# Optimization experiments

Hardware: AMD Instinct MI355X
Metric: run time of the kernel (lower is better)

The kernel has to match this reference:

```python
import jax, jax.numpy as jnp
import numpy as np
import math

D_MODEL = 1024
N_HEADS = 16
HEAD_DIM = D_MODEL // N_HEADS
FEAT = 16
WINDOW = 64
EPS_NORM = 1e-6
EPS_LIN = 1e-6
CHUNK = 128


def setup_inputs() -> dict:
    key = jax.random.key(0)
    ks = jax.random.split(key, 7)
    B, T = 2, 2048
    s = 0.02
    return {
        'x': jax.random.normal(ks[0], (B, T, D_MODEL), jnp.float32),
        'norm_w': jnp.ones((D_MODEL,), jnp.float32),
        'Wq': jax.random.normal(ks[1], (D_MODEL, D_MODEL), jnp.float32) * s,
        'Wk': jax.random.normal(ks[2], (D_MODEL, D_MODEL), jnp.float32) * s,
        'Wv': jax.random.normal(ks[3], (D_MODEL, D_MODEL), jnp.float32) * s,
        'Wqf': jax.random.normal(ks[4], (HEAD_DIM, FEAT), jnp.float32) * s,
        'Wkf': jax.random.normal(ks[5], (HEAD_DIM, FEAT), jnp.float32) * s,
        'Wout': jax.random.normal(ks[6], (2 * D_MODEL, D_MODEL), jnp.float32) * s,
    }


def rmsnorm(x, w):
    return x * jax.lax.rsqrt(jnp.mean(x * x, axis=-1, keepdims=True) + EPS_NORM) * w


def taylor_feature_map(x):
    # phi(x) = [1, x, x_i*x_j * (0.5 if i==j else 1/sqrt(2)) for i<=j]
    d = x.shape[-1]
    iu, ju = jnp.triu_indices(d)  # row-major (i, j>=i) matches torch loop order
    scale = jnp.where(iu == ju, 0.5, 1.0 / math.sqrt(2.0)).astype(x.dtype)
    quad = x[..., iu] * x[..., ju] * scale
    ones = jnp.ones(x.shape[:-1] + (1,), dtype=x.dtype)
    return jnp.concatenate([ones, x, quad], axis=-1)  # (..., 1+d+d(d+1)/2)


def linear_attention_causal(q_phi, k_phi, v):
    # Chunked-parallel causal linear attention: y_t = q_t @ KV_t / (q_t @ Ksum_t + eps)
    B, T, H, F = q_phi.shape
    D = v.shape[-1]
    Nc = T // CHUNK
    qc = q_phi.reshape(B, Nc, CHUNK, H, F).transpose(1, 0, 2, 3, 4)  # (Nc,B,C,H,F)
    kc = k_phi.reshape(B, Nc, CHUNK, H, F).transpose(1, 0, 2, 3, 4)
    vc = v.reshape(B, Nc, CHUNK, H, D).transpose(1, 0, 2, 3, 4)      # (Nc,B,C,H,D)
    causal = jnp.tril(jnp.ones((CHUNK, CHUNK), dtype=q_phi.dtype))   # include diagonal

    def step(carry, inp):
        kv, ksum = carry                      # (B,H,F,D), (B,H,F)
        qb, kb, vb = inp
        A = jnp.einsum('bchf,bshf->bhcs', qb, kb) * causal  # intra-chunk quadratic scores
        y = jnp.einsum('bhcs,bshd->bchd', A, vb) + jnp.einsum('bchf,bhfd->bchd', qb, kv)
        z = jnp.einsum('bhcs->bch', A) + jnp.einsum('bchf,bhf->bch', qb, ksum)
        kv = kv + jnp.einsum('bshf,bshd->bhfd', kb, vb)
        ksum = ksum + kb.sum(axis=1)
        return (kv, ksum), y / (z[..., None] + EPS_LIN)

    kv0 = jnp.zeros((B, H, F, D), dtype=q_phi.dtype)
    ks0 = jnp.zeros((B, H, F), dtype=q_phi.dtype)
    _, ys = jax.lax.scan(step, (kv0, ks0), (qc, kc, vc))
    return ys.transpose(1, 0, 2, 3, 4).reshape(B, T, H, D)


def sliding_window_attention(q, k, v):
    B, T, H, D = q.shape
    scale = 1.0 / math.sqrt(D)
    t = jnp.arange(T)
    allowed = (t[None, :] <= t[:, None]) & (t[None, :] >= t[:, None] - WINDOW)  # (T,T)
    scores = jnp.einsum('bqhd,bkhd->bhqk', q, k) * scale
    scores = jnp.where(allowed[None, None], scores, -jnp.inf)
    attn = jax.nn.softmax(scores, axis=-1)
    out = jnp.einsum('bhqk,bkhd->bqhd', attn, v)
    return out.reshape(B, T, H * D)


def reference(x, norm_w, Wq, Wk, Wv, Wqf, Wkf, Wout):
    B, T, _ = x.shape
    h = rmsnorm(x, norm_w)
    q = (h @ Wq).reshape(B, T, N_HEADS, HEAD_DIM)
    k = (h @ Wk).reshape(B, T, N_HEADS, HEAD_DIM)
    v = (h @ Wv).reshape(B, T, N_HEADS, HEAD_DIM)
    q_phi = taylor_feature_map(q @ Wqf)
    k_phi = taylor_feature_map(k @ Wkf)
    lin = linear_attention_causal(q_phi, k_phi, v).reshape(B, T, D_MODEL)
    win = sliding_window_attention(q, k, v)
    out = jnp.concatenate([lin, win], axis=-1) @ Wout
    return x + out
```

## Files before the change

kernel.cpp:

```cpp
#include <hip/hip_runtime.h>
#include <math.h>

#define BB 2
#define TT 2048
#define DM 1024
#define NH 16
#define HD 64
#define FEAT 16
#define WIN 64
#define RTOT (BB*TT)

typedef __bf16 bf16x8 __attribute__((ext_vector_type(8)));
typedef float  f32x4  __attribute__((ext_vector_type(4)));

__device__ __forceinline__ unsigned short f2bf(float f) {
    union { float f; unsigned u; } v; v.f = f;
    unsigned r = v.u + 0x7FFFu + ((v.u >> 16) & 1u);
    return (unsigned short)(r >> 16);
}
__device__ __forceinline__ float bf2f(unsigned short u) {
    union { unsigned u; float f; } v; v.u = ((unsigned)u) << 16; return v.f;
}

__device__ __forceinline__ void gl2lds16(const void* g, void* l) {
    __builtin_amdgcn_global_load_lds(
        (const __attribute__((address_space(1))) void*)g,
        (__attribute__((address_space(3))) void*)l, 16, 0, 0);
}

__global__ __launch_bounds__(256) void rmsnorm_kernel(const float* __restrict__ x,
                                                      const float* __restrict__ w,
                                                      unsigned short* __restrict__ h_bf) {
    int row = blockIdx.x;
    int tid = threadIdx.x;
    const float4* xr = (const float4*)(x + (size_t)row * DM);
    float4 xv = xr[tid];
    float ss = xv.x*xv.x + xv.y*xv.y + xv.z*xv.z + xv.w*xv.w;
    #pragma unroll
    for (int off = 32; off > 0; off >>= 1) ss += __shfl_down(ss, off, 64);
    __shared__ float red[4];
    if ((tid & 63) == 0) red[tid >> 6] = ss;
    __syncthreads();
    float tot = red[0] + red[1] + red[2] + red[3];
    float scale = rsqrtf(tot * (1.0f / DM) + 1e-6f);
    float4 wv = ((const float4*)w)[tid];
    ushort4 o;
    o.x = f2bf(xv.x * scale * wv.x);
    o.y = f2bf(xv.y * scale * wv.y);
    o.z = f2bf(xv.z * scale * wv.z);
    o.w = f2bf(xv.w * scale * wv.w);
    *(ushort4*)&h_bf[(size_t)row * DM + tid * 4] = o;
}

__global__ __launch_bounds__(256) void transpose_bf16_kernel(const float* __restrict__ W0,
                                                             const float* __restrict__ W1,
                                                             const float* __restrict__ W2,
                                                             const float* __restrict__ W3,
                                                             unsigned short* __restrict__ T0,
                                                             unsigned short* __restrict__ T1,
                                                             unsigned short* __restrict__ T2,
                                                             unsigned short* __restrict__ T3) {
    int z = blockIdx.z;
    int K = (z == 3) ? 2048 : 1024;
    const int N = 1024;
    if (blockIdx.y * 64 >= K) return;
    const float* W = (z == 0) ? W0 : (z == 1) ? W1 : (z == 2) ? W2 : W3;
    unsigned short* WT = (z == 0) ? T0 : (z == 1) ? T1 : (z == 2) ? T2 : T3;
    __shared__ float tile[64][65];
    int k0 = blockIdx.y * 64, n0 = blockIdx.x * 64;
    int t = threadIdx.x;
    int r = t >> 4, c4 = (t & 15) * 4;
    #pragma unroll
    for (int i = 0; i < 4; i++) {
        float4 vv = *(const float4*)&W[(size_t)(k0 + r + i*16) * N + n0 + c4];
        tile[r + i*16][c4 + 0] = vv.x;
        tile[r + i*16][c4 + 1] = vv.y;
        tile[r + i*16][c4 + 2] = vv.z;
        tile[r + i*16][c4 + 3] = vv.w;
    }
    __syncthreads();
    int rn = t >> 2, kq = (t & 3) * 16;
    unsigned short u[16];
    #pragma unroll
    for (int i = 0; i < 16; i++) u[i] = f2bf(tile[kq + i][rn]);
    size_t base = (size_t)(n0 + rn) * K + k0 + kq;
    *(uint4*)&WT[base]     = *(uint4*)&u[0];
    *(uint4*)&WT[base + 8] = *(uint4*)&u[8];
}

template<int LD, int NT>
__device__ __forceinline__ void gemm2h_core(const unsigned short* __restrict__ A,
                                            const unsigned short* __restrict__ BT,
                                            unsigned short* __restrict__ Cb,
                                            int k0g) {
    const int N = 1024;
    __shared__ __align__(16) unsigned short L[2][4][256 * 32];
    int tid = threadIdx.x;
    int lane = tid & 63;
    int w = tid >> 6;
    int wm = (w >> 2) * 128, wn = (w & 3) * 64;
    int m0 = blockIdx.y * 256, n0 = blockIdx.x * 256;
    int hi = lane >> 4;
    int l15 = lane & 15;

    int c0 = tid, c1 = tid + 512;
    int r0 = c0 >> 2, kh0 = ((c0 & 3) - (r0 >> 1)) & 3;
    int r1 = c1 >> 2, kh1 = ((c1 & 3) - (r1 >> 1)) & 3;
    const unsigned short* aS0 = A  + (size_t)(m0 + r0) * LD + k0g + kh0 * 8;
    const unsigned short* aS1 = A  + (size_t)(m0 + r1) * LD + k0g + kh1 * 8;
    const unsigned short* bS0 = BT + (size_t)(n0 + r0) * LD + k0g + kh0 * 8;
    const unsigned short* bS1 = BT + (size_t)(n0 + r1) * LD + k0g + kh1 * 8;

    int aoff[8], boff[4];
    #pragma unroll
    for (int i = 0; i < 8; i++) {
        int m = wm + i * 16 + l15;
        aoff[i] = m * 32 + (((hi + (m >> 1)) & 3) * 8);
    }
    #pragma unroll
    for (int j = 0; j < 4; j++) {
        int n = wn + j * 16 + l15;
        boff[j] = n * 32 + (((hi + (n >> 1)) & 3) * 8);
    }

    f32x4 acc[8][4];
    #pragma unroll
    for (int i = 0; i < 8; i++)
        #pragma unroll
        for (int j = 0; j < 4; j++)
            acc[i][j] = (f32x4){0.f, 0.f, 0.f, 0.f};

#define STG8(kt, bf, rg) do {                                         \
        int _go = (kt) * 64 + ((rg) >> 1) * 32;                       \
        unsigned short* _d = &L[bf][rg][0];                           \
        if ((rg) & 1) { gl2lds16(bS0 + _go, _d + c0 * 8);             \
                        gl2lds16(bS1 + _go, _d + c1 * 8); }           \
        else          { gl2lds16(aS0 + _go, _d + c0 * 8);             \
                        gl2lds16(aS1 + _go, _d + c1 * 8); }           \
    } while (0)

    STG8(0, 0, 0); STG8(0, 0, 1); STG8(0, 0, 2); STG8(0, 0, 3);
    asm volatile("s_waitcnt vmcnt(4)" ::: "memory");
    __builtin_amdgcn_s_barrier();

    for (int t = 0; t < NT; t++) {
        int rd = t & 1, st = rd ^ 1;
        bool stg = (t + 1 < NT);
        const unsigned short* A0 = &L[rd][0][0];
        const unsigned short* B0 = &L[rd][1][0];
        const unsigned short* A1 = &L[rd][2][0];
        const unsigned short* B1 = &L[rd][3][0];
        bf16x8 af[8], bfr[4];

        asm volatile("" ::: "memory");
        #pragma unroll
        for (int i = 0; i < 8; i++) af[i] = *(const bf16x8*)&A0[aoff[i]];
        #pragma unroll
        for (int j = 0; j < 4; j++) bfr[j] = *(const bf16x8*)&B0[boff[j]];
        if (stg) { STG8(t + 1, st, 0); STG8(t + 1, st, 1); }
        __builtin_amdgcn_s_setprio(1);
        #pragma unroll
        for (int i = 0; i < 8; i++)
            #pragma unroll
            for (int j = 0; j < 4; j++)
                acc[i][j] = __builtin_amdgcn_mfma_f32_16x16x32_bf16(af[i], bfr[j], acc[i][j], 0, 0, 0);
        __builtin_amdgcn_s_setprio(0);
        if (stg) {
            asm volatile("s_waitcnt vmcnt(4)" ::: "memory");
        } else {
            asm volatile("s_waitcnt vmcnt(0)" ::: "memory");
        }
        __builtin_amdgcn_s_barrier();

        asm volatile("" ::: "memory");
        #pragma unroll
        for (int i = 0; i < 8; i++) af[i] = *(const bf16x8*)&A1[aoff[i]];
        #pragma unroll
        for (int j = 0; j < 4; j++) bfr[j] = *(const bf16x8*)&B1[boff[j]];
        if (stg) { STG8(t + 1, st, 2); STG8(t + 1, st, 3); }
        __builtin_amdgcn_s_setprio(1);
        #pragma unroll
        for (int i = 0; i < 8; i++)
            #pragma unroll
            for (int j = 0; j < 4; j++)
                acc[i][j] = __builtin_amdgcn_mfma_f32_16x16x32_bf16(af[i], bfr[j], acc[i][j], 0, 0, 0);
        __builtin_amdgcn_s_setprio(0);
        if (stg) {
            asm volatile("s_waitcnt vmcnt(4)" ::: "memory");
            __builtin_amdgcn_s_barrier();
        }
    }
#undef STG8

    #pragma unroll
    for (int i = 0; i < 8; i++) {
        #pragma unroll
        for (int j = 0; j < 4; j++) {
            int col = n0 + wn + j * 16 + l15;
            #pragma unroll
            for (int r = 0; r < 4; r++) {
                int row = m0 + wm + i * 16 + hi * 4 + r;
                Cb[(size_t)row * N + col] = f2bf(acc[i][j][r]);
            }
        }
    }
}

__global__ __launch_bounds__(512, 2) void gemm_qkv_mfma(const unsigned short* __restrict__ A,
                                                        const unsigned short* __restrict__ BT0,
                                                        const unsigned short* __restrict__ BT1,
                                                        const unsigned short* __restrict__ BT2,
                                                        unsigned short* __restrict__ C0,
                                                        unsigned short* __restrict__ C1,
                                                        unsigned short* __restrict__ C2) {
    const unsigned short* BT = (blockIdx.z == 0) ? BT0 : (blockIdx.z == 1) ? BT1 : BT2;
    unsigned short* C = (blockIdx.z == 0) ? C0 : (blockIdx.z == 1) ? C1 : C2;
    gemm2h_core<1024, 16>(A, BT, C, 0);
}

__global__ __launch_bounds__(512, 2) void gemm_out_mfma(const unsigned short* __restrict__ A,
                                                        const unsigned short* __restrict__ BT,
                                                        unsigned short* __restrict__ P0,
                                                        unsigned short* __restrict__ P1,
                                                        unsigned short* __restrict__ P2,
                                                        unsigned short* __restrict__ P3) {
    unsigned short* P = (blockIdx.z == 0) ? P0 : (blockIdx.z == 1) ? P1
                      : (blockIdx.z == 2) ? P2 : P3;
    gemm2h_core<2048, 8>(A, BT, P, blockIdx.z * 512);
}

__global__ __launch_bounds__(256) void out_reduce_kernel(const float* __restrict__ x,
                                                         const unsigned short* __restrict__ P0,
                                                         const unsigned short* __restrict__ P1,
                                                         const unsigned short* __restrict__ P2,
                                                         const unsigned short* __restrict__ P3,
                                                         float* __restrict__ out) {
    int g = blockIdx.x * 256 + threadIdx.x;
    size_t e = (size_t)g * 4;
    float4 xv = *(const float4*)&x[e];
    ushort4 a = *(const ushort4*)&P0[e];
    ushort4 b = *(const ushort4*)&P1[e];
    ushort4 c = *(const ushort4*)&P2[e];
    ushort4 d = *(const ushort4*)&P3[e];
    float4 o;
    o.x = xv.x + bf2f(a.x) + bf2f(b.x) + bf2f(c.x) + bf2f(d.x);
    o.y = xv.y + bf2f(a.y) + bf2f(b.y) + bf2f(c.y) + bf2f(d.y);
    o.z = xv.z + bf2f(a.z) + bf2f(b.z) + bf2f(c.z) + bf2f(d.z);
    o.w = xv.w + bf2f(a.w) + bf2f(b.w) + bf2f(c.w) + bf2f(d.w);
    *(float4*)&out[e] = o;
}

__global__ __launch_bounds__(256) void feat_kernel(const unsigned short* __restrict__ qb,
                                                   const unsigned short* __restrict__ kb,
                                                   const float* __restrict__ Wqf,
                                                   const float* __restrict__ Wkf,
                                                   unsigned short* __restrict__ qf,
                                                   unsigned short* __restrict__ kf) {
    __shared__ float Wl[HD * FEAT];
    const unsigned short* src = blockIdx.z ? kb : qb;
    const float* Wm = blockIdx.z ? Wkf : Wqf;
    unsigned short* dst = blockIdx.z ? kf : qf;
    int tid = threadIdx.x;
    ((float4*)Wl)[tid] = ((const float4*)Wm)[tid];
    __syncthreads();
    int gid = blockIdx.x * 256 + tid;
    int f = gid & 15;
    int rowh = gid >> 4;
    const unsigned short* s = src + (size_t)rowh * HD;
    float acc = 0.f;
    #pragma unroll
    for (int d = 0; d < HD; d++) acc += bf2f(s[d]) * Wl[d * FEAT + f];
    dst[gid] = f2bf(acc);
}

__global__ __launch_bounds__(256) void win_mfma_kernel(const unsigned short* __restrict__ q_bf,
                                                       const unsigned short* __restrict__ k_bf,
                                                       const unsigned short* __restrict__ v_bf,
                                                       unsigned short* __restrict__ cat_bf) {
    int qtile = blockIdx.x;
    int bh = blockIdx.y;
    int h = bh & 15;
    int b = bh >> 4;
    int tid = threadIdx.x;
    int lane = tid & 63;
    int wv = tid >> 6;
    int qr0 = wv * 16;
    int t0 = qtile * 64;
    int k0 = t0 - 64;

    __shared__ __align__(16) unsigned short Qs[64 * 64];
    __shared__ __align__(16) unsigned short Ks[128 * 64];
    __shared__ __align__(16) unsigned short Vt[64 * 128];
    __shared__ __align__(16) unsigned short Pl[64 * 128];

    #pragma unroll
    for (int half = 0; half < 2; half++) {
        int slot = tid + half * 256;
        int row = slot >> 3, pos = slot & 7;
        int o = (pos - row) & 7;
        gl2lds16(q_bf + (size_t)(b * TT + t0 + row) * (NH * HD) + h * HD + o * 8,
                 &Qs[slot * 8]);
    }
    #pragma unroll
    for (int qd = 0; qd < 4; qd++) {
        int slot = tid + qd * 256;
        int row = slot >> 3, pos = slot & 7;
        int o = (pos - row) & 7;
        int kg = k0 + row;
        if (kg >= 0) {
            gl2lds16(k_bf + (size_t)(b * TT + kg) * (NH * HD) + h * HD + o * 8,
                     &Ks[slot * 8]);
        } else {
            uint4 z = {0, 0, 0, 0};
            *(uint4*)&Ks[slot * 8] = z;
        }
    }
    {
        int kk = tid & 127;
        int dh = tid >> 7;
        int kg = k0 + kk;
        unsigned short tmp[32];
        if (kg >= 0) {
            size_t base = (size_t)(b * TT + kg) * (NH * HD) + h * HD + dh * 32;
            *(uint4*)&tmp[0]  = *(const uint4*)&v_bf[base];
            *(uint4*)&tmp[8]  = *(const uint4*)&v_bf[base + 8];
            *(uint4*)&tmp[16] = *(const uint4*)&v_bf[base + 16];
            *(uint4*)&tmp[24] = *(const uint4*)&v_bf[base + 24];
        } else {
            #pragma unroll
            for (int d = 0; d < 32; d++) tmp[d] = 0;
        }
        int o = kk >> 3, klow = kk & 7;
        #pragma unroll
        for (int d = 0; d < 32; d++) {
            int dim = dh * 32 + d;
            Vt[dim * 128 + ((o + dim) & 15) * 8 + klow] = tmp[d];
        }
    }
    __syncthreads();

    int hi = lane >> 4;
    int lan15 = lane & 15;
    f32x4 sc[8];
    #pragma unroll
    for (int nt = 0; nt < 8; nt++) sc[nt] = (f32x4){0.f, 0.f, 0.f, 0.f};
    #pragma unroll
    for (int ks = 0; ks < 2; ks++) {
        int m = qr0 + lan15;
        int oA = ks * 4 + hi;
        bf16x8 a = *(const bf16x8*)&Qs[m * 64 + ((oA + m) & 7) * 8];
        #pragma unroll
        for (int nt = 0; nt < 8; nt++) {
            int n = nt * 16 + lan15;
            bf16x8 bb = *(const bf16x8*)&Ks[n * 64 + ((oA + n) & 7) * 8];
            sc[nt] = __builtin_amdgcn_mfma_f32_16x16x32_bf16(a, bb, sc[nt], 0, 0, 0);
        }
    }

    float lrow[4];
    #pragma unroll
    for (int r = 0; r < 4; r++) {
        int tq = t0 + qr0 + hi * 4 + r;
        float mx = -1e30f;
        #pragma unroll
        for (int nt = 0; nt < 8; nt++) {
            int s = k0 + nt * 16 + lan15;
            bool ok = (s >= 0) && (s <= tq) && (s >= tq - WIN);
            float vv = ok ? sc[nt][r] * 0.125f : -1e30f;
            sc[nt][r] = vv;
            mx = fmaxf(mx, vv);
        }
        #pragma unroll
        for (int off = 1; off < 16; off <<= 1) mx = fmaxf(mx, __shfl_xor(mx, off, 64));
        float ls = 0.f;
        #pragma unroll
        for (int nt = 0; nt < 8; nt++) {
            float e = __expf(sc[nt][r] - mx);
            sc[nt][r] = e;
            ls += e;
        }
        #pragma unroll
        for (int off = 1; off < 16; off <<= 1) ls += __shfl_xor(ls, off, 64);
        lrow[r] = ls;
    }

    #pragma unroll
    for (int nt = 0; nt < 8; nt++) {
        #pragma unroll
        for (int r = 0; r < 4; r++) {
            int row = qr0 + hi * 4 + r;
            int col = nt * 16 + lan15;
            Pl[row * 128 + (((col >> 3) + row) & 15) * 8 + (col & 7)] = f2bf(sc[nt][r]);
        }
    }
    __syncthreads();

    f32x4 y[4];
    #pragma unroll
    for (int nt = 0; nt < 4; nt++) y[nt] = (f32x4){0.f, 0.f, 0.f, 0.f};
    #pragma unroll
    for (int ks = 0; ks < 4; ks++) {
        int m = qr0 + lan15;
        int oA = ks * 4 + hi;
        bf16x8 a = *(const bf16x8*)&Pl[m * 128 + ((oA + m) & 15) * 8];
        #pragma unroll
        for (int nt = 0; nt < 4; nt++) {
            int n = nt * 16 + lan15;
            bf16x8 bb = *(const bf16x8*)&Vt[n * 128 + ((oA + n) & 15) * 8];
            y[nt] = __builtin_amdgcn_mfma_f32_16x16x32_bf16(a, bb, y[nt], 0, 0, 0);
        }
    }

    #pragma unroll
    for (int nt = 0; nt < 4; nt++) {
        #pragma unroll
        for (int r = 0; r < 4; r++) {
            int row = qr0 + hi * 4 + r;
            int dim = nt * 16 + lan15;
            cat_bf[(size_t)(b * TT + t0 + row) * (2 * DM) + DM + h * HD + dim] =
                f2bf(y[nt][r] / lrow[r]);
        }
    }
}

#define PHI 160
#define NCH 32
#define KVROWS 65
#define CH_STRIDE ((size_t)32 * KVROWS * PHI)

__global__ __launch_bounds__(256) void lin_kv_kernel(const unsigned short* __restrict__ kf,
                                                     const unsigned short* __restrict__ v_bf,
                                                     unsigned short* __restrict__ kvbuf) {
    int c = blockIdx.x, bh = blockIdx.y;
    int h = bh & 15, b = bh >> 4;
    int tid = threadIdx.x, lane = tid & 63, w = tid >> 6;
    int hi = lane >> 4, l15 = lane & 15;

    __shared__ unsigned short kf_l[64 * 16];
    __shared__ __align__(16) unsigned short PhiT[192 * 76];
    __shared__ __align__(16) unsigned short Vt[80 * 64];
    __shared__ unsigned short iu[136], ju[136];
    __shared__ float sclut[136];

    if (tid < 136) {
        int qq = tid, i = 0;
        while (qq >= 16 - i) { qq -= 16 - i; i++; }
        iu[tid] = (unsigned short)i; ju[tid] = (unsigned short)(i + qq);
        sclut[tid] = (qq == 0) ? 0.5f : 0.70710678118654752f;
    }
    {
        int r = tid >> 2, f4 = (tid & 3) * 4;
        *(ushort4*)&kf_l[r * 16 + f4] =
            *(const ushort4*)&kf[((size_t)((b * TT + c * 64 + r) * NH + h)) * FEAT + f4];
    }
    {
        int p = tid & 31, dq = (tid >> 5) * 8;
        size_t base0 = ((size_t)(b * TT + c * 64 + 2 * p)) * DM + h * HD + dq;
        unsigned short a[8], bq[8];
        *(uint4*)a  = *(const uint4*)&v_bf[base0];
        *(uint4*)bq = *(const uint4*)&v_bf[base0 + DM];
        int colo = p >> 2, coll = (2 * p) & 7;
        #pragma unroll
        for (int d = 0; d < 8; d++) {
            int row = dq + d;
            ushort2 u; u.x = a[d]; u.y = bq[d];
            *(ushort2*)&Vt[row * 64 + ((colo + row) & 7) * 8 + coll] = u;
        }
        #pragma unroll
        for (int i = 0; i < 4; i++) {
            int e = tid + i * 256;
            Vt[(64 + (e >> 6)) * 64 + (e & 63)] = 0x3F80;
        }
    }
    __syncthreads();
    {
        int s = tid & 63, fb = tid >> 6;
        const unsigned short* krow = &kf_l[s * 16];
        for (int it = 0; it < 40; it++) {
            int f = fb * 40 + it;
            float val;
            if (f == 0) val = 1.f;
            else if (f < 17) val = bf2f(krow[f - 1]);
            else if (f < 153) { int qq = f - 17; val = bf2f(krow[iu[qq]]) * bf2f(krow[ju[qq]]) * sclut[qq]; }
            else val = 0.f;
            PhiT[f * 76 + s] = f2bf(val);
        }
    }
    __syncthreads();
    f32x4 acc[5][3];
    #pragma unroll
    for (int m = 0; m < 5; m++)
        #pragma unroll
        for (int j = 0; j < 3; j++) acc[m][j] = (f32x4){0.f, 0.f, 0.f, 0.f};
    #pragma unroll
    for (int ks = 0; ks < 2; ks++) {
        bf16x8 bfrag[3];
        #pragma unroll
        for (int j = 0; j < 3; j++)
            bfrag[j] = *(const bf16x8*)&PhiT[((3 * w + j) * 16 + l15) * 76 + ks * 32 + hi * 8];
        #pragma unroll
        for (int m = 0; m < 5; m++) {
            int mrow = m * 16 + l15;
            bf16x8 afrag = *(const bf16x8*)&Vt[mrow * 64 + (((ks * 4 + hi) + mrow) & 7) * 8];
            #pragma unroll
            for (int j = 0; j < 3; j++)
                acc[m][j] = __builtin_amdgcn_mfma_f32_16x16x32_bf16(afrag, bfrag[j], acc[m][j], 0, 0, 0);
        }
    }
    size_t obase = ((size_t)c * 32 + bh) * (KVROWS * PHI);
    #pragma unroll
    for (int m = 0; m < 5; m++) {
        #pragma unroll
        for (int j = 0; j < 3; j++) {
            int f = (3 * w + j) * 16 + l15;
            if (f >= PHI) continue;
            #pragma unroll
            for (int r = 0; r < 4; r++) {
                int row = m * 16 + hi * 4 + r;
                if (row >= KVROWS) continue;
                kvbuf[obase + row * PHI + f] = f2bf(acc[m][j][r]);
            }
        }
    }
}

__global__ __launch_bounds__(256) void lin_scan_kernel(unsigned short* __restrict__ kvbuf) {
    int e = blockIdx.x * 256 + threadIdx.x;
    int bh = blockIdx.y;
    if (e >= KVROWS * PHI) return;
    float acc = 0.f;
    size_t off = (size_t)bh * (KVROWS * PHI) + e;
    for (int c = 0; c < NCH; c++) {
        float vv = bf2f(kvbuf[off]);
        kvbuf[off] = f2bf(acc);
        acc += vv;
        off += CH_STRIDE;
    }
}

__global__ __launch_bounds__(256) void lin_out_kernel(const unsigned short* __restrict__ qf,
                                                      const unsigned short* __restrict__ kf,
                                                      const unsigned short* __restrict__ v_bf,
                                                      const unsigned short* __restrict__ kvbuf,
                                                      unsigned short* __restrict__ cat_bf) {
    int c = blockIdx.x, bh = blockIdx.y;
    int h = bh & 15, b = bh >> 4;
    int tid = threadIdx.x, lane = tid & 63, w = tid >> 6;
    int hi = lane >> 4, l15 = lane & 15;

    __shared__ unsigned short qf_l[64 * 16];
    __shared__ __align__(16) unsigned short kf_lb[64 * 34];
    __shared__ __align__(16) unsigned short KVS_l[80 * 164];
    __shared__ __align__(16) unsigned short Vt[80 * 64];
    __shared__ __align__(16) unsigned short Phi_l[64 * 164];
    __shared__ __align__(16) unsigned short P_l[64 * 64];
    __shared__ unsigned short iu[136], ju[136];
    __shared__ float sclut[136];

    if (tid < 136) {
        int qq = tid, i = 0;
        while (qq >= 16 - i) { qq -= 16 - i; i++; }
        iu[tid] = (unsigned short)i; ju[tid] = (unsigned short)(i + qq);
        sclut[tid] = (qq == 0) ? 0.5f : 0.70710678118654752f;
    }
    {
        int r = tid >> 2, f4 = (tid & 3) * 4;
        *(ushort4*)&qf_l[r * 16 + f4] =
            *(const ushort4*)&qf[((size_t)((b * TT + c * 64 + r) * NH + h)) * FEAT + f4];
    }
    {
        int r = tid >> 2, f4 = (tid & 3) * 4;
        *(ushort4*)&kf_lb[r * 34 + f4] =
            *(const ushort4*)&kf[((size_t)((b * TT + c * 64 + r) * NH + h)) * FEAT + f4];
        ushort4 z4 = {0, 0, 0, 0};
        *(ushort4*)&kf_lb[r * 34 + 16 + f4] = z4;
    }
    {
        int p = tid & 31, dq = (tid >> 5) * 8;
        size_t base0 = ((size_t)(b * TT + c * 64 + 2 * p)) * DM + h * HD + dq;
        unsigned short a[8], bq[8];
        *(uint4*)a  = *(const uint4*)&v_bf[base0];
        *(uint4*)bq = *(const uint4*)&v_bf[base0 + DM];
        int colo = p >> 2, coll = (2 * p) & 7;
        #pragma unroll
        for (int d = 0; d < 8; d++) {
            int row = dq + d;
            ushort2 u; u.x = a[d]; u.y = bq[d];
            *(ushort2*)&Vt[row * 64 + ((colo + row) & 7) * 8 + coll] = u;
        }
        #pragma unroll
        for (int i = 0; i < 4; i++) {
            int e = tid + i * 256;
            Vt[(64 + (e >> 6)) * 64 + (e & 63)] = 0x3F80;
        }
    }
    {
        size_t gbase = ((size_t)c * 32 + bh) * (KVROWS * PHI);
        #pragma unroll
        for (int i = 0; i < 11; i++) {
            int e4 = tid + i * 256;
            if (e4 < KVROWS * 40) {
                int r = e4 / 40, q4 = (e4 % 40) * 4;
                *(ushort4*)&KVS_l[r * 164 + q4] =
                    *(const ushort4*)&kvbuf[gbase + r * PHI + q4];
            }
        }
        #pragma unroll
        for (int i = 0; i < 3; i++) {
            int e4 = tid + i * 256;
            if (e4 < 15 * 40) {
                int r = 65 + e4 / 40, q4 = (e4 % 40) * 4;
                ushort4 z4 = {0, 0, 0, 0};
                *(ushort4*)&KVS_l[r * 164 + q4] = z4;
            }
        }
    }
    __syncthreads();

    {
        int s = tid & 63, fb = tid >> 6;
        const unsigned short* qrow = &qf_l[s * 16];
        for (int it = 0; it < 40; it++) {
            int f = fb * 40 + it;
            float val;
            if (f == 0) val = 1.f;
            else if (f < 17) val = bf2f(qrow[f - 1]);
            else if (f < 153) { int qq = f - 17; val = bf2f(qrow[iu[qq]]) * bf2f(qrow[ju[qq]]) * sclut[qq]; }
            else val = 0.f;
            Phi_l[s * 164 + f] = f2bf(val);
        }
    }
    __syncthreads();

    f32x4 acc[5];
    #pragma unroll
    for (int n = 0; n < 5; n++) acc[n] = (f32x4){0.f, 0.f, 0.f, 0.f};

    int t_m = w * 16 + l15;

    #pragma unroll
    for (int ks = 0; ks < 5; ks++) {
        bf16x8 af = *(const bf16x8*)&Phi_l[t_m * 164 + ks * 32 + hi * 8];
        #pragma unroll
        for (int n = 0; n < 5; n++) {
            bf16x8 bb = *(const bf16x8*)&KVS_l[(n * 16 + l15) * 164 + ks * 32 + hi * 8];
            acc[n] = __builtin_amdgcn_mfma_f32_16x16x32_bf16(af, bb, acc[n], 0, 0, 0);
        }
    }

    {
        union { unsigned short u[8]; bf16x8 v; } aq;
        #pragma unroll
        for (int j = 0; j < 8; j++) {
            int f = hi * 8 + j;
            aq.u[j] = (f < 16) ? qf_l[t_m * 16 + f] : (unsigned short)0;
        }
        #pragma unroll
        for (int n = 0; n < 4; n++) {
            bf16x8 bk = *(const bf16x8*)&kf_lb[(n * 16 + l15) * 34 + hi * 8];
            f32x4 zv = {0.f, 0.f, 0.f, 0.f};
            f32x4 sc = __builtin_amdgcn_mfma_f32_16x16x32_bf16(aq.v, bk, zv, 0, 0, 0);
            int sl = n * 16 + l15;
            #pragma unroll
            for (int r = 0; r < 4; r++) {
                int rl = w * 16 + hi * 4 + r;
                float sv = 1.f + 0.5f * sc[r];
                sv = sv * sv;
                if (sl > rl) sv = 0.f;
                P_l[rl * 64 + (((sl >> 3) + rl) & 7) * 8 + (sl & 7)] = f2bf(sv);
            }
        }
    }
    __syncthreads();

    #pragma unroll
    for (int ks = 0; ks < 2; ks++) {
        int oA = ks * 4 + hi;
        bf16x8 a = *(const bf16x8*)&P_l[t_m * 64 + ((oA + t_m) & 7) * 8];
        #pragma unroll
        for (int n = 0; n < 5; n++) {
            int nrow = n * 16 + l15;
            bf16x8 bb = *(const bf16x8*)&Vt[nrow * 64 + ((oA + nrow) & 7) * 8];
            acc[n] = __builtin_amdgcn_mfma_f32_16x16x32_bf16(a, bb, acc[n], 0, 0, 0);
        }
    }

    #pragma unroll
    for (int r = 0; r < 4; r++) {
        float zz = __shfl(acc[4][r], (lane & 48), 64);
        int token = c * 64 + w * 16 + hi * 4 + r;
        #pragma unroll
        for (int n = 0; n < 4; n++) {
            int d = n * 16 + l15;
            cat_bf[((size_t)(b * TT + token)) * (2 * DM) + h * HD + d] =
                f2bf(acc[n][r] / (zz + 1e-6f));
        }
    }
}

extern "C" void kernel_launch(void* const* d_in, const int* in_sizes, int n_in,
                              void* d_out, int out_size, void* d_ws, size_t ws_size,
                              hipStream_t stream) {
    const float* x      = (const float*)d_in[0];
    const float* norm_w = (const float*)d_in[1];
    const float* Wq     = (const float*)d_in[2];
    const float* Wk     = (const float*)d_in[3];
    const float* Wv     = (const float*)d_in[4];
    const float* Wqf    = (const float*)d_in[5];
    const float* Wkf    = (const float*)d_in[6];
    const float* Wout   = (const float*)d_in[7];
    float* out = (float*)d_out;

    char* p = (char*)d_ws;
    unsigned short* h_bf = (unsigned short*)p; p += (size_t)RTOT * DM * 2;
    unsigned short* WqT  = (unsigned short*)p; p += (size_t)DM * DM * 2;
    unsigned short* WkT  = (unsigned short*)p; p += (size_t)DM * DM * 2;
    unsigned short* WvT  = (unsigned short*)p; p += (size_t)DM * DM * 2;
    unsigned short* WoT  = (unsigned short*)p; p += (size_t)DM * 2 * DM * 2;
    unsigned short* q_bf = (unsigned short*)p; p += (size_t)RTOT * DM * 2;
    unsigned short* k_bf = (unsigned short*)p; p += (size_t)RTOT * DM * 2;
    unsigned short* v_bf = (unsigned short*)p; p += (size_t)RTOT * DM * 2;
    unsigned short* qf_bf = (unsigned short*)p; p += (size_t)RTOT * NH * FEAT * 2;
    unsigned short* kf_bf = (unsigned short*)p; p += (size_t)RTOT * NH * FEAT * 2;
    unsigned short* cat_bf = (unsigned short*)p; p += (size_t)RTOT * 2 * DM * 2;
    unsigned short* kvbuf  = (unsigned short*)p; p += (size_t)NCH * 32 * KVROWS * PHI * 2;
    unsigned short* P0 = (unsigned short*)p; p += (size_t)RTOT * DM * 2;
    unsigned short* P1 = (unsigned short*)p; p += (size_t)RTOT * DM * 2;
    unsigned short* P2 = h_bf;
    unsigned short* P3 = q_bf;

    rmsnorm_kernel<<<RTOT, 256, 0, stream>>>(x, norm_w, h_bf);
    transpose_bf16_kernel<<<dim3(16, 32, 4), 256, 0, stream>>>(Wq, Wk, Wv, Wout, WqT, WkT, WvT, WoT);
    gemm_qkv_mfma<<<dim3(4, 16, 3), 512, 0, stream>>>(h_bf, WqT, WkT, WvT, q_bf, k_bf, v_bf);
    feat_kernel<<<dim3((RTOT * NH * FEAT) / 256, 1, 2), 256, 0, stream>>>(q_bf, k_bf, Wqf, Wkf, qf_bf, kf_bf);
    win_mfma_kernel<<<dim3(TT / 64, BB * NH), 256, 0, stream>>>(q_bf, k_bf, v_bf, cat_bf);
    lin_kv_kernel<<<dim3(NCH, BB * NH), 256, 0, stream>>>(kf_bf, v_bf, kvbuf);
    lin_scan_kernel<<<dim3((KVROWS * PHI + 255) / 256, BB * NH), 256, 0, stream>>>(kvbuf);
    lin_out_kernel<<<dim3(NCH, BB * NH), 256, 0, stream>>>(qf_bf, kf_bf, v_bf, kvbuf, cat_bf);
    gemm_out_mfma<<<dim3(4, 16, 4), 512, 0, stream>>>(cat_bf, WoT, P0, P1, P2, P3);
    out_reduce_kernel<<<RTOT * DM / 1024, 256, 0, stream>>>(x, P0, P1, P2, P3, out);
}
```

Baseline: 250.2 us.

## Fuse feature projection into linear-attention kernels and merge norm with weight transpose

Measured after the change: 246.6 us. About the same (-1.4%).

```diff
diff --git a/kernel.cpp b/kernel.cpp
--- a/kernel.cpp
+++ b/kernel.cpp
@@ -28,48 +28,53 @@
         (__attribute__((address_space(3))) void*)l, 16, 0, 0);
 }
 
-__global__ __launch_bounds__(256) void rmsnorm_kernel(const float* __restrict__ x,
-                                                      const float* __restrict__ w,
-                                                      unsigned short* __restrict__ h_bf) {
-    int row = blockIdx.x;
+__global__ __launch_bounds__(256) void prep_kernel(const float* __restrict__ x,
+                                                   const float* __restrict__ w,
+                                                   unsigned short* __restrict__ h_bf,
+                                                   const float* __restrict__ W0,
+                                                   const float* __restrict__ W1,
+                                                   const float* __restrict__ W2,
+                                                   const float* __restrict__ W3,
+                                                   unsigned short* __restrict__ T0,
+                                                   unsigned short* __restrict__ T1,
+                                                   unsigned short* __restrict__ T2,
+                                                   unsigned short* __restrict__ T3) {
+    __shared__ float red[4];
+    __shared__ float tile[64][65];
+    int bx = blockIdx.x;
     int tid = threadIdx.x;
-    const float4* xr = (const float4*)(x + (size_t)row * DM);
-    float4 xv = xr[tid];
-    float ss = xv.x*xv.x + xv.y*xv.y + xv.z*xv.z + xv.w*xv.w;
-    #pragma unroll
-    for (int off = 32; off > 0; off >>= 1) ss += __shfl_down(ss, off, 64);
-    __shared__ float red[4];
-    if ((tid & 63) == 0) red[tid >> 6] = ss;
-    __syncthreads();
-    float tot = red[0] + red[1] + red[2] + red[3];
-    float scale = rsqrtf(tot * (1.0f / DM) + 1e-6f);
-    float4 wv = ((const float4*)w)[tid];
-    ushort4 o;
-    o.x = f2bf(xv.x * scale * wv.x);
-    o.y = f2bf(xv.y * scale * wv.y);
-    o.z = f2bf(xv.z * scale * wv.z);
-    o.w = f2bf(xv.w * scale * wv.w);
-    *(ushort4*)&h_bf[(size_t)row * DM + tid * 4] = o;
-}
-
-__global__ __launch_bounds__(256) void transpose_bf16_kernel(const float* __restrict__ W0,
-                                                             const float* __restrict__ W1,
-                                                             const float* __restrict__ W2,
-                                                             const float* __restrict__ W3,
-                                                             unsigned short* __restrict__ T0,
-                                                             unsigned short* __restrict__ T1,
-                                                             unsigned short* __restrict__ T2,
-                                                             unsigned short* __restrict__ T3) {
-    int z = blockIdx.z;
+    if (bx < RTOT) {
+        int row = bx;
+        const float4* xr = (const float4*)(x + (size_t)row * DM);
+        float4 xv = xr[tid];
+        float ss = xv.x*xv.x + xv.y*xv.y + xv.z*xv.z + xv.w*xv.w;
+        #pragma unroll
+        for (int off = 32; off > 0; off >>= 1) ss += __shfl_down(ss, off, 64);
+        if ((tid & 63) == 0) red[tid >> 6] = ss;
+        __syncthreads();
+        float tot = red[0] + red[1] + red[2] + red[3];
+        float scale = rsqrtf(tot * (1.0f / DM) + 1e-6f);
+        float4 wv = ((const float4*)w)[tid];
+        ushort4 o;
+        o.x = f2bf(xv.x * scale * wv.x);
+        o.y = f2bf(xv.y * scale * wv.y);
+        o.z = f2bf(xv.z * scale * wv.z);
+        o.w = f2bf(xv.w * scale * wv.w);
+        *(ushort4*)&h_bf[(size_t)row * DM + tid * 4] = o;
+        return;
+    }
+    int t = bx - RTOT;
+    int z = t >> 9;
+    int rem = t & 511;
+    int by = rem >> 4;
+    int bxx = rem & 15;
     int K = (z == 3) ? 2048 : 1024;
     const int N = 1024;
-    if (blockIdx.y * 64 >= K) return;
+    if (by * 64 >= K) return;
     const float* W = (z == 0) ? W0 : (z == 1) ? W1 : (z == 2) ? W2 : W3;
     unsigned short* WT = (z == 0) ? T0 : (z == 1) ? T1 : (z == 2) ? T2 : T3;
-    __shared__ float tile[64][65];
-    int k0 = blockIdx.y * 64, n0 = blockIdx.x * 64;
-    int t = threadIdx.x;
-    int r = t >> 4, c4 = (t & 15) * 4;
+    int k0 = by * 64, n0 = bxx * 64;
+    int r = tid >> 4, c4 = (tid & 15) * 4;
     #pragma unroll
     for (int i = 0; i < 4; i++) {
         float4 vv = *(const float4*)&W[(size_t)(k0 + r + i*16) * N + n0 + c4];
@@ -79,7 +84,7 @@
         tile[r + i*16][c4 + 3] = vv.w;
     }
     __syncthreads();
-    int rn = t >> 2, kq = (t & 3) * 16;
+    int rn = tid >> 2, kq = (tid & 3) * 16;
     unsigned short u[16];
     #pragma unroll
     for (int i = 0; i < 16; i++) u[i] = f2bf(tile[kq + i][rn]);
@@ -250,29 +255,6 @@
     *(float4*)&out[e] = o;
 }
 
-__global__ __launch_bounds__(256) void feat_kernel(const unsigned short* __restrict__ qb,
-                                                   const unsigned short* __restrict__ kb,
-                                                   const float* __restrict__ Wqf,
-                                                   const float* __restrict__ Wkf,
-                                                   unsigned short* __restrict__ qf,
-                                                   unsigned short* __restrict__ kf) {
-    __shared__ float Wl[HD * FEAT];
-    const unsigned short* src = blockIdx.z ? kb : qb;
-    const float* Wm = blockIdx.z ? Wkf : Wqf;
-    unsigned short* dst = blockIdx.z ? kf : qf;
-    int tid = threadIdx.x;
-    ((float4*)Wl)[tid] = ((const float4*)Wm)[tid];
-    __syncthreads();
-    int gid = blockIdx.x * 256 + tid;
-    int f = gid & 15;
-    int rowh = gid >> 4;
-    const unsigned short* s = src + (size_t)rowh * HD;
-    float acc = 0.f;
-    #pragma unroll
-    for (int d = 0; d < HD; d++) acc += bf2f(s[d]) * Wl[d * FEAT + f];
-    dst[gid] = f2bf(acc);
-}
-
 __global__ __launch_bounds__(256) void win_mfma_kernel(const unsigned short* __restrict__ q_bf,
                                                        const unsigned short* __restrict__ k_bf,
                                                        const unsigned short* __restrict__ v_bf,
@@ -428,7 +410,8 @@
 #define KVROWS 65
 #define CH_STRIDE ((size_t)32 * KVROWS * PHI)
 
-__global__ __launch_bounds__(256) void lin_kv_kernel(const unsigned short* __restrict__ kf,
+__global__ __launch_bounds__(256) void lin_kv_kernel(const unsigned short* __restrict__ k_bf,
+                                                     const float* __restrict__ Wkf,
                                                      const unsigned short* __restrict__ v_bf,
                                                      unsigned short* __restrict__ kvbuf) {
     int c = blockIdx.x, bh = blockIdx.y;
@@ -442,6 +425,9 @@
     __shared__ unsigned short iu[136], ju[136];
     __shared__ float sclut[136];
 
+    unsigned short* ks_l = &PhiT[0];
+    float* Wf = (float*)&PhiT[4096];
+
     if (tid < 136) {
         int qq = tid, i = 0;
         while (qq >= 16 - i) { qq -= 16 - i; i++; }
@@ -449,10 +435,12 @@
         sclut[tid] = (qq == 0) ? 0.5f : 0.70710678118654752f;
     }
     {
-        int r = tid >> 2, f4 = (tid & 3) * 4;
-        *(ushort4*)&kf_l[r * 16 + f4] =
-            *(const ushort4*)&kf[((size_t)((b * TT + c * 64 + r) * NH + h)) * FEAT + f4];
-    }
+        int r = tid >> 2, q16 = (tid & 3) * 16;
+        size_t gb = ((size_t)(b * TT + c * 64 + r)) * DM + h * HD + q16;
+        *(uint4*)&ks_l[r * 64 + q16]     = *(const uint4*)&k_bf[gb];
+        *(uint4*)&ks_l[r * 64 + q16 + 8] = *(const uint4*)&k_bf[gb + 8];
+    }
+    ((float4*)Wf)[tid] = ((const float4*)Wkf)[tid];
     {
         int p = tid & 31, dq = (tid >> 5) * 8;
         size_t base0 = ((size_t)(b * TT + c * 64 + 2 * p)) * DM + h * HD + dq;
@@ -471,6 +459,20 @@
             int e = tid + i * 256;
             Vt[(64 + (e >> 6)) * 64 + (e & 63)] = 0x3F80;
         }
+    }
+    __syncthreads();
+    {
+        int r = tid >> 2, f0 = (tid & 3) * 4;
+        const unsigned short* kr = &ks_l[r * 64];
+        float a0 = 0.f, a1 = 0.f, a2 = 0.f, a3 = 0.f;
+        #pragma unroll 8
+        for (int d = 0; d < HD; d++) {
+            float kv = bf2f(kr[d]);
+            const float* wr = &Wf[d * FEAT + f0];
+            a0 += kv * wr[0]; a1 += kv * wr[1]; a2 += kv * wr[2]; a3 += kv * wr[3];
+        }
+        ushort4 o; o.x = f2bf(a0); o.y = f2bf(a1); o.z = f2bf(a2); o.w = f2bf(a3);
+        *(ushort4*)&kf_l[r * 16 + f0] = o;
     }
     __syncthreads();
     {
@@ -538,8 +540,10 @@
     }
 }
 
-__global__ __launch_bounds__(256) void lin_out_kernel(const unsigned short* __restrict__ qf,
-                                                      const unsigned short* __restrict__ kf,
+__global__ __launch_bounds__(256) void lin_out_kernel(const unsigned short* __restrict__ q_bf,
+                                                      const unsigned short* __restrict__ k_bf,
+                                                      const float* __restrict__ Wqf,
+                                                      const float* __restrict__ Wkf,
                                                       const unsigned short* __restrict__ v_bf,
                                                       const unsigned short* __restrict__ kvbuf,
                                                       unsigned short* __restrict__ cat_bf) {
@@ -557,6 +561,11 @@
     __shared__ unsigned short iu[136], ju[136];
     __shared__ float sclut[136];
 
+    unsigned short* qs_l = &KVS_l[0];
+    unsigned short* ks_l = &KVS_l[64 * 64];
+    float* Wq_s = (float*)&Phi_l[0];
+    float* Wk_s = (float*)&Phi_l[2048];
+
     if (tid < 136) {
         int qq = tid, i = 0;
         while (qq >= 16 - i) { qq -= 16 - i; i++; }
@@ -564,17 +573,15 @@
         sclut[tid] = (qq == 0) ? 0.5f : 0.70710678118654752f;
     }
     {
-        int r = tid >> 2, f4 = (tid & 3) * 4;
-        *(ushort4*)&qf_l[r * 16 + f4] =
-            *(const ushort4*)&qf[((size_t)((b * TT + c * 64 + r) * NH + h)) * FEAT + f4];
-    }
-    {
-        int r = tid >> 2, f4 = (tid & 3) * 4;
-        *(ushort4*)&kf_lb[r * 34 + f4] =
-            *(const ushort4*)&kf[((size_t)((b * TT + c * 64 + r) * NH + h)) * FEAT + f4];
-        ushort4 z4 = {0, 0, 0, 0};
-        *(ushort4*)&kf_lb[r * 34 + 16 + f4] = z4;
-    }
+        int r = tid >> 2, q16 = (tid & 3) * 16;
+        size_t gq = ((size_t)(b * TT + c * 64 + r)) * DM + h * HD + q16;
+        *(uint4*)&qs_l[r * 64 + q16]     = *(const uint4*)&q_bf[gq];
+        *(uint4*)&qs_l[r * 64 + q16 + 8] = *(const uint4*)&q_bf[gq + 8];
+        *(uint4*)&ks_l[r * 64 + q16]     = *(const uint4*)&k_bf[gq];
+        *(uint4*)&ks_l[r * 64 + q16 + 8] = *(const uint4*)&k_bf[gq + 8];
+    }
+    ((float4*)Wq_s)[tid] = ((const float4*)Wqf)[tid];
+    ((float4*)Wk_s)[tid] = ((const float4*)Wkf)[tid];
     {
         int p = tid & 31, dq = (tid >> 5) * 8;
         size_t base0 = ((size_t)(b * TT + c * 64 + 2 * p)) * DM + h * HD + dq;
@@ -594,6 +601,29 @@
             Vt[(64 + (e >> 6)) * 64 + (e & 63)] = 0x3F80;
         }
     }
+    __syncthreads();
+    {
+        int r = tid >> 2, f0 = (tid & 3) * 4;
+        const unsigned short* qr = &qs_l[r * 64];
+        const unsigned short* kr = &ks_l[r * 64];
+        float qa0=0.f,qa1=0.f,qa2=0.f,qa3=0.f, ka0=0.f,ka1=0.f,ka2=0.f,ka3=0.f;
+        #pragma unroll 8
+        for (int d = 0; d < HD; d++) {
+            float qv = bf2f(qr[d]);
+            float kv = bf2f(kr[d]);
+            const float* wq = &Wq_s[d * FEAT + f0];
+            const float* wk = &Wk_s[d * FEAT + f0];
+            qa0 += qv * wq[0]; qa1 += qv * wq[1]; qa2 += qv * wq[2]; qa3 += qv * wq[3];
+            ka0 += kv * wk[0]; ka1 += kv * wk[1]; ka2 += kv * wk[2]; ka3 += kv * wk[3];
+        }
+        ushort4 oq; oq.x = f2bf(qa0); oq.y = f2bf(qa1); oq.z = f2bf(qa2); oq.w = f2bf(qa3);
+        ushort4 ok; ok.x = f2bf(ka0); ok.y = f2bf(ka1); ok.z = f2bf(ka2); ok.w = f2bf(ka3);
+        *(ushort4*)&qf_l[r * 16 + f0] = oq;
+        *(ushort4*)&kf_lb[r * 34 + f0] = ok;
+        ushort4 z4 = {0, 0, 0, 0};
+        *(ushort4*)&kf_lb[r * 34 + 16 + f0] = z4;
+    }
+    __syncthreads();
     {
         size_t gbase = ((size_t)c * 32 + bh) * (KVROWS * PHI);
         #pragma unroll
@@ -615,8 +645,6 @@
             }
         }
     }
-    __syncthreads();
-
     {
         int s = tid & 63, fb = tid >> 6;
         const unsigned short* qrow = &qf_l[s * 16];
@@ -720,8 +748,7 @@
     unsigned short* q_bf = (unsigned short*)p; p += (size_t)RTOT * DM * 2;
     unsigned short* k_bf = (unsigned short*)p; p += (size_t)RTOT * DM * 2;
     unsigned short* v_bf = (unsigned short*)p; p += (size_t)RTOT * DM * 2;
-    unsigned short* qf_bf = (unsigned short*)p; p += (size_t)RTOT * NH * FEAT * 2;
-    unsigned short* kf_bf = (unsigned short*)p; p += (size_t)RTOT * NH * FEAT * 2;
+    p += (size_t)RTOT * NH * FEAT * 2 * 2;
     unsigned short* cat_bf = (unsigned short*)p; p += (size_t)RTOT * 2 * DM * 2;
     unsigned short* kvbuf  = (unsigned short*)p; p += (size_t)NCH * 32 * KVROWS * PHI * 2;
     unsigned short* P0 = (unsigned short*)p; p += (size_t)RTOT * DM * 2;
@@ -729,14 +756,13 @@
     unsigned short* P2 = h_bf;
     unsigned short* P3 = q_bf;
 
-    rmsnorm_kernel<<<RTOT, 256, 0, stream>>>(x, norm_w, h_bf);
-    transpose_bf16_kernel<<<dim3(16, 32, 4), 256, 0, stream>>>(Wq, Wk, Wv, Wout, WqT, WkT, WvT, WoT);
+    prep_kernel<<<RTOT + 2048, 256, 0, stream>>>(x, norm_w, h_bf,
+                                                 Wq, Wk, Wv, Wout, WqT, WkT, WvT, WoT);
     gemm_qkv_mfma<<<dim3(4, 16, 3), 512, 0, stream>>>(h_bf, WqT, WkT, WvT, q_bf, k_bf, v_bf);
-    feat_kernel<<<dim3((RTOT * NH * FEAT) / 256, 1, 2), 256, 0, stream>>>(q_bf, k_bf, Wqf, Wkf, qf_bf, kf_bf);
     win_mfma_kernel<<<dim3(TT / 64, BB * NH), 256, 0, stream>>>(q_bf, k_bf, v_bf, cat_bf);
-    lin_kv_kernel<<<dim3(NCH, BB * NH), 256, 0, stream>>>(kf_bf, v_bf, kvbuf);
+    lin_kv_kernel<<<dim3(NCH, BB * NH), 256, 0, stream>>>(k_bf, Wkf, v_bf, kvbuf);
     lin_scan_kernel<<<dim3((KVROWS * PHI + 255) / 256, BB * NH), 256, 0, stream>>>(kvbuf);
-    lin_out_kernel<<<dim3(NCH, BB * NH), 256, 0, stream>>>(qf_bf, kf_bf, v_bf, kvbuf, cat_bf);
+    lin_out_kernel<<<dim3(NCH, BB * NH), 256, 0, stream>>>(q_bf, k_bf, Wqf, Wkf, v_bf, kvbuf, cat_bf);
     gemm_out_mfma<<<dim3(4, 16, 4), 512, 0, stream>>>(cat_bf, WoT, P0, P1, P2, P3);
     out_reduce_kernel<<<RTOT * DM / 1024, 256, 0, stream>>>(x, P0, P1, P2, P3, out);
 }
```
